# Kernel tuning notes

Hardware: AMD Instinct MI355X
Metric: run time of the kernel (lower is better)

## Reference

```python
import jax, jax.numpy as jnp
import numpy as np

N = 50000      # nodes
E = 500000     # edges (avg degree 10)
G = 64         # graphs (events)
IN = 7
H = 64
EPS = 1e-5


def setup_inputs() -> dict:
    key = jax.random.key(0)
    ks = iter(jax.random.split(key, 64))
    d = {}
    d["x"] = jax.random.normal(next(ks), (N, IN), jnp.float32)
    d["edge_index"] = jax.random.randint(next(ks), (2, E), 0, N, dtype=jnp.int32)
    d["batch"] = jnp.sort(jax.random.randint(next(ks), (N,), 0, G, dtype=jnp.int32))
    dims = [(IN, H), (H, 2 * H), (2 * H, 4 * H)]
    for i, (ic, oc) in enumerate(dims, 1):
        d[f"b{i}_W1"] = jax.random.normal(next(ks), (2 * ic, oc), jnp.float32) * 0.05
        d[f"b{i}_b1"] = jnp.zeros((oc,), jnp.float32)
        d[f"b{i}_g1"] = jnp.ones((oc,), jnp.float32)
        d[f"b{i}_beta1"] = jnp.zeros((oc,), jnp.float32)
        d[f"b{i}_W2"] = jax.random.normal(next(ks), (oc, oc), jnp.float32) * 0.05
        d[f"b{i}_b2"] = jnp.zeros((oc,), jnp.float32)
        d[f"b{i}_g2"] = jnp.ones((oc,), jnp.float32)
        d[f"b{i}_beta2"] = jnp.zeros((oc,), jnp.float32)
    d["head_W1"] = jax.random.normal(next(ks), (4 * H, 2 * H), jnp.float32) * 0.05
    d["head_b1"] = jnp.zeros((2 * H,), jnp.float32)
    d["head_W2"] = jax.random.normal(next(ks), (2 * H, 2), jnp.float32) * 0.05
    d["head_b2"] = jnp.zeros((2,), jnp.float32)
    return d


def _bn(h, g, b):
    # BatchNorm1d in training mode: batch statistics over edge dim
    m = h.mean(axis=0)
    v = h.var(axis=0)
    return (h - m) * jax.lax.rsqrt(v + EPS) * g + b


def _edgeconv(x, src, dst, W1, b1, g1, be1, W2, b2, g2, be2):
    # PyG EdgeConv: message = MLP(cat[x_i, x_j - x_i]), aggregated at target i=dst
    xi = x[dst]                                   # [E, C]
    xj = x[src]                                   # [E, C]
    e = jnp.concatenate([xi, xj - xi], axis=-1)   # [E, 2C]
    h = jax.nn.relu(_bn(e @ W1 + b1, g1, be1))
    h = jax.nn.relu(_bn(h @ W2 + b2, g2, be2))
    s = jax.ops.segment_sum(h, dst, num_segments=N)
    cnt = jax.ops.segment_sum(jnp.ones((h.shape[0],), h.dtype), dst, num_segments=N)
    return s / jnp.maximum(cnt, 1.0)[:, None]     # mean aggregation


def reference(x, edge_index, batch,
              b1_W1, b1_b1, b1_g1, b1_beta1, b1_W2, b1_b2, b1_g2, b1_beta2,
              b2_W1, b2_b1, b2_g1, b2_beta1, b2_W2, b2_b2, b2_g2, b2_beta2,
              b3_W1, b3_b1, b3_g1, b3_beta1, b3_W2, b3_b2, b3_g2, b3_beta2,
              head_W1, head_b1, head_W2, head_b2):
    src, dst = edge_index[0], edge_index[1]
    h = _edgeconv(x, src, dst, b1_W1, b1_b1, b1_g1, b1_beta1, b1_W2, b1_b2, b1_g2, b1_beta2)
    h = _edgeconv(h, src, dst, b2_W1, b2_b1, b2_g1, b2_beta1, b2_W2, b2_b2, b2_g2, b2_beta2)
    h = _edgeconv(h, src, dst, b3_W1, b3_b1, b3_g1, b3_beta1, b3_W2, b3_b2, b3_g2, b3_beta2)
    # global mean pool per graph
    s = jax.ops.segment_sum(h, batch, num_segments=G)
    cnt = jax.ops.segment_sum(jnp.ones((N,), h.dtype), batch, num_segments=G)
    g = s / jnp.maximum(cnt, 1.0)[:, None]        # [G, 256]
    # head (dropout is identity in eval)
    z = jax.nn.relu(g @ head_W1 + head_b1)
    return z @ head_W2 + head_b2                  # [G, 2]
```

## Files before the change

### kernel.cpp

```cpp
#include <hip/hip_runtime.h>
#include <stdint.h>

constexpr int NN = 50000;
constexpr int NE = 500000;
constexpr int NG = 64;
constexpr float BN_EPS = 1e-5f;

typedef __attribute__((ext_vector_type(8))) short bf16x8;
typedef __attribute__((ext_vector_type(4))) float f32x4;

__device__ inline float bf2f(unsigned short u) {
    return __uint_as_float(((unsigned int)u) << 16);
}
__device__ inline unsigned short f2bf_rne(float f) {
    unsigned int u = __float_as_uint(f);
    unsigned int r = (u + 0x7fffu + ((u >> 16) & 1u)) >> 16;
    return (unsigned short)r;
}

template<int CPT> __device__ inline void load_row(const float* p, float* o) {
    if constexpr (CPT == 2) { float2 v = *(const float2*)p; o[0]=v.x; o[1]=v.y; }
    else if constexpr (CPT == 4) { float4 v = *(const float4*)p; o[0]=v.x; o[1]=v.y; o[2]=v.z; o[3]=v.w; }
    else { load_row<4>(p, o); load_row<4>(p+4, o+4); }
}
template<int CPT> __device__ inline void store_row(float* p, const float* v) {
    if constexpr (CPT == 2) { *(float2*)p = make_float2(v[0], v[1]); }
    else if constexpr (CPT == 4) { *(float4*)p = make_float4(v[0], v[1], v[2], v[3]); }
    else { store_row<4>(p, v); store_row<4>(p+4, v+4); }
}

__global__ void k_zero16(uint4* p, int n) {
    int i = blockIdx.x * 256 + threadIdx.x;
    if (i < n) p[i] = uint4{0u, 0u, 0u, 0u};
}

__global__ void k_diag(float* out, int n, float val) {
    int i = blockIdx.x * 256 + threadIdx.x;
    if (i < n) out[i] = val;
}

__global__ void k_deg(const int* __restrict__ dst, int* __restrict__ degi) {
    int e = blockIdx.x * 256 + threadIdx.x;
    if (e < NE) atomicAdd(&degi[dst[e]], 1);
}

__global__ void k_scan(const int* __restrict__ degi, int* __restrict__ rowptr) {
    __shared__ int buf[1024];
    __shared__ int carry_s;
    const int tid = threadIdx.x;
    if (tid == 0) carry_s = 0;
    __syncthreads();
    for (int base = 0; base < NN; base += 1024) {
        int i = base + tid;
        int v = (i < NN) ? degi[i] : 0;
        buf[tid] = v;
        __syncthreads();
        for (int off = 1; off < 1024; off <<= 1) {
            int t = (tid >= off) ? buf[tid - off] : 0;
            __syncthreads();
            buf[tid] += t;
            __syncthreads();
        }
        if (i < NN) rowptr[i] = carry_s + buf[tid] - v;
        __syncthreads();
        if (tid == 0) carry_s += buf[1023];
        __syncthreads();
    }
    if (tid == 0) rowptr[NN] = carry_s;
}

__global__ void k_fill(const int* __restrict__ dst, const int* __restrict__ rowptr,
                       int* __restrict__ cursor, int* __restrict__ eidx) {
    int e = blockIdx.x * 256 + threadIdx.x;
    if (e < NE) {
        int d = dst[e];
        int p = atomicAdd(&cursor[d], 1);
        eidx[rowptr[d] + p] = e;
    }
}

__global__ void k_grange(const int* __restrict__ batch, int* __restrict__ gse) {
    int n = blockIdx.x * 256 + threadIdx.x;
    if (n >= NN) return;
    int b = batch[n];
    if (n == 0 || batch[n-1] != b) gse[b] = n;
    if (n == NN-1 || batch[n+1] != b) gse[NG + b] = n + 1;
}

template<int OC>
__global__ void k_bnfin(const float* __restrict__ st, const float* __restrict__ g,
                        const float* __restrict__ be, float* __restrict__ dv) {
    int c = threadIdx.x;
    const float invE = 1.0f / (float)NE;
    float m = st[c] * invE;
    float v = st[OC + c] * invE - m * m;
    float sc = g[c] * rsqrtf(v + BN_EPS);
    dv[c] = sc;
    dv[OC + c] = be[c] - m * sc;
}

template<int OC>
__global__ void k_packW(const float* __restrict__ W,
                        unsigned short* __restrict__ Wph, unsigned short* __restrict__ Wpl) {
    constexpr int NT = OC / 16;
    const int l = threadIdx.x;
    const int ktnt = blockIdx.x;
    const int n = (ktnt % NT) * 16 + (l & 15);
    const int kbase = (ktnt / NT) * 32 + (l >> 4) * 8;
    size_t fo = ((size_t)ktnt * 64 + l) * 8;
    #pragma unroll
    for (int b = 0; b < 8; b++) {
        float w = W[(size_t)(kbase + b) * OC + n];
        unsigned short h = f2bf_rne(w);
        Wph[fo + b] = h;
        Wpl[fo + b] = f2bf_rne(w - bf2f(h));
    }
}

template<int CIN, int OC>
__global__ __launch_bounds__(256) void k_nodeproj(
    const float* __restrict__ x, const float* __restrict__ W1,
    const float* __restrict__ b1, float* __restrict__ A, float* __restrict__ Bn)
{
    constexpr int SP = CIN + 1;
    constexpr int CPT = OC / 32;
    __shared__ float xs[32 * SP];
    const int t = threadIdx.x;
    const int n0 = blockIdx.x * 32;
    {
        const int el = t >> 3, l8 = t & 7;
        int n = n0 + el; if (n >= NN) n = NN - 1;
        const float* xp = x + (size_t)n * CIN;
        for (int k = l8; k < CIN; k += 8) xs[el * SP + k] = xp[k];
    }
    __syncthreads();
    const int tx = t & 31, ty = t >> 5;
    float accA[4][CPT], accB[4][CPT];
    #pragma unroll
    for (int i = 0; i < 4; i++)
        #pragma unroll
        for (int j = 0; j < CPT; j++) { accA[i][j] = 0.f; accB[i][j] = 0.f; }

    const float* Wa = W1 + tx * CPT;
    const float* Wb = W1 + (size_t)CIN * OC + tx * CPT;
    for (int k = 0; k < CIN; k++) {
        float wa[CPT], wb[CPT];
        load_row<CPT>(Wa + (size_t)k * OC, wa);
        load_row<CPT>(Wb + (size_t)k * OC, wb);
        #pragma unroll
        for (int i = 0; i < 4; i++) {
            float ev = xs[(ty * 4 + i) * SP + k];
            #pragma unroll
            for (int j = 0; j < CPT; j++) {
                accA[i][j] = fmaf(ev, wa[j] - wb[j], accA[i][j]);
                accB[i][j] = fmaf(ev, wb[j], accB[i][j]);
            }
        }
    }
    float bs[CPT];
    load_row<CPT>(b1 + tx * CPT, bs);
    #pragma unroll
    for (int i = 0; i < 4; i++) {
        const int n = n0 + ty * 4 + i;
        if (n < NN) {
            float va[CPT];
            #pragma unroll
            for (int j = 0; j < CPT; j++) va[j] = accA[i][j] + bs[j];
            store_row<CPT>(A  + (size_t)n * OC + tx * CPT, va);
            store_row<CPT>(Bn + (size_t)n * OC + tx * CPT, accB[i]);
        }
    }
}

template<int OC>
__global__ __launch_bounds__(256) void k_stats1(
    const float* __restrict__ A, const float* __restrict__ Bn,
    const int* __restrict__ src, const int* __restrict__ dst,
    const int* __restrict__ eidx, float* __restrict__ stats)
{
    constexpr int CPT = OC / 32;
    __shared__ float reds[4 * OC];
    __shared__ float redq[4 * OC];
    const int t = threadIdx.x;
    const int l32 = t & 31, grp = t >> 5;
    float s[CPT], q[CPT];
    #pragma unroll
    for (int j = 0; j < CPT; j++) { s[j] = 0.f; q[j] = 0.f; }
    for (int i = blockIdx.x * 8 + grp; i < NE; i += 8192) {
        const int e = eidx[i];
        float av[CPT], bv[CPT];
        load_row<CPT>(A  + (size_t)dst[e] * OC + l32 * CPT, av);
        load_row<CPT>(Bn + (size_t)src[e] * OC + l32 * CPT, bv);
        #pragma unroll
        for (int j = 0; j < CPT; j++) {
            float h = av[j] + bv[j];
            s[j] += h; q[j] += h * h;
        }
    }
    #pragma unroll
    for (int j = 0; j < CPT; j++) {
        s[j] += __shfl_down(s[j], 32);
        q[j] += __shfl_down(q[j], 32);
    }
    const int w = t >> 6, lane = t & 63;
    if (lane < 32) {
        #pragma unroll
        for (int j = 0; j < CPT; j++) {
            reds[w * OC + lane * CPT + j] = s[j];
            redq[w * OC + lane * CPT + j] = q[j];
        }
    }
    __syncthreads();
    for (int c = t; c < OC; c += 256) {
        float S = reds[c] + reds[OC + c] + reds[2 * OC + c] + reds[3 * OC + c];
        float Q = redq[c] + redq[OC + c] + redq[2 * OC + c] + redq[3 * OC + c];
        atomicAdd(&stats[c], S);
        atomicAdd(&stats[OC + c], Q);
    }
}

template<int OC, int MODE>
__global__ __launch_bounds__(512, 3) void k_efuse(
    const float* __restrict__ A, const float* __restrict__ Bn,
    const int* __restrict__ src, const int* __restrict__ dst,
    const int* __restrict__ eidx,
    const unsigned short* __restrict__ Wph, const unsigned short* __restrict__ Wpl,
    const float* __restrict__ b2,
    const float* __restrict__ dv1, float* __restrict__ stats,
    const float* __restrict__ dv2, float* __restrict__ xout)
{
    constexpr int ETL = 128;
    constexpr int NT = OC / 16;
    constexpr int NTW = NT / 4;
    constexpr int NCH = OC / 64;
    constexpr int SROWS = 8192 / OC;
    constexpr int NSTRIP = ETL / SROWS;
    constexpr int YSTR = OC + 4;
    constexpr int YB = SROWS * YSTR * 4;
    constexpr int TB = (MODE == 0) ? 16384 : 32768;
    constexpr int SMB = (MODE == 1 && YB > TB) ? YB : TB;
    constexpr int NSEG = 512 / OC;
    constexpr int RSEG = SROWS / NSEG;

    __shared__ __align__(16) unsigned char smem[SMB];
    __shared__ int sdst_s[ETL], ssrc_s[ETL];

    const int t = threadIdx.x;
    const int e0 = blockIdx.x * ETL;
    const int valid = (NE - e0 < ETL) ? (NE - e0) : ETL;

    if (t < ETL) {
        int dn = -1, sn = -1;
        if (t < valid) { int e = eidx[e0 + t]; dn = dst[e]; sn = src[e]; }
        sdst_s[t] = dn; ssrc_s[t] = sn;
    }
    __syncthreads();

    const int lane = t & 63, wave = t >> 6;
    const int rg = wave >> 2, ch = wave & 3;
    const int lr = lane & 15, lg = lane >> 4;

    f32x4 acc[4][NTW];
    #pragma unroll
    for (int m = 0; m < 4; m++)
        #pragma unroll
        for (int n = 0; n < NTW; n++) acc[m][n] = (f32x4){0.f, 0.f, 0.f, 0.f};

    const int brow = t >> 2, q = t & 3;
    const bool rvalid = (brow < valid);
    const float* Arow = rvalid ? (A  + (size_t)sdst_s[brow] * OC + q * 16) : nullptr;
    const float* Brow = rvalid ? (Bn + (size_t)ssrc_s[brow] * OC + q * 16) : nullptr;

    for (int kc = 0; kc < NCH; kc++) {
        {
            const int gc0 = kc * 64 + q * 16;
            if (rvalid) {
                #pragma unroll
                for (int i = 0; i < 4; i++) {
                    float4 a  = *(const float4*)(Arow + kc * 64 + i * 4);
                    float4 b  = *(const float4*)(Brow + kc * 64 + i * 4);
                    float4 sc = *(const float4*)(dv1 + gc0 + i * 4);
                    float4 sh = *(const float4*)(dv1 + OC + gc0 + i * 4);
                    float tv[4];
                    tv[0] = fmaxf(fmaf(a.x + b.x, sc.x, sh.x), 0.f);
                    tv[1] = fmaxf(fmaf(a.y + b.y, sc.y, sh.y), 0.f);
                    tv[2] = fmaxf(fmaf(a.z + b.z, sc.z, sh.z), 0.f);
                    tv[3] = fmaxf(fmaf(a.w + b.w, sc.w, sh.w), 0.f);
                    unsigned short hv[4];
                    #pragma unroll
                    for (int j = 0; j < 4; j++) hv[j] = f2bf_rne(tv[j]);
                    const int byt = (brow * 128 + q * 32 + i * 8) ^ ((brow & 7) << 4);
                    *(ushort4*)(smem + byt) = *(ushort4*)hv;
                    if constexpr (MODE == 1) {
                        unsigned short lv[4];
                        #pragma unroll
                        for (int j = 0; j < 4; j++) lv[j] = f2bf_rne(tv[j] - bf2f(hv[j]));
                        *(ushort4*)(smem + 16384 + byt) = *(ushort4*)lv;
                    }
                }
            } else {
                const ushort4 z = ushort4{0, 0, 0, 0};
                #pragma unroll
                for (int i = 0; i < 4; i++) {
                    const int byt = (brow * 128 + q * 32 + i * 8) ^ ((brow & 7) << 4);
                    *(ushort4*)(smem + byt) = z;
                    if constexpr (MODE == 1) *(ushort4*)(smem + 16384 + byt) = z;
                }
            }
        }
        __syncthreads();

        #pragma unroll
        for (int kt2 = 0; kt2 < 2; kt2++) {
            bf16x8 ah[4], al[4];
            #pragma unroll
            for (int m = 0; m < 4; m++) {
                const int r = rg * 64 + m * 16 + lr;
                const int byt = (r * 128 + kt2 * 64 + lg * 16) ^ ((r & 7) << 4);
                ah[m] = *(const bf16x8*)(smem + byt);
                if constexpr (MODE == 1) al[m] = *(const bf16x8*)(smem + 16384 + byt);
            }
            #pragma unroll
            for (int n = 0; n < NTW; n++) {
                const size_t fo = ((size_t)((kc * 2 + kt2) * NT + ch * NTW + n) * 64 + lane) * 8;
                bf16x8 wh = *(const bf16x8*)(Wph + fo);
                if constexpr (MODE == 0) {
                    #pragma unroll
                    for (int m = 0; m < 4; m++)
                        acc[m][n] = __builtin_amdgcn_mfma_f32_16x16x32_bf16(ah[m], wh, acc[m][n], 0, 0, 0);
                } else {
                    bf16x8 wl = *(const bf16x8*)(Wpl + fo);
                    #pragma unroll
                    for (int m = 0; m < 4; m++) {
                        acc[m][n] = __builtin_amdgcn_mfma_f32_16x16x32_bf16(ah[m], wh, acc[m][n], 0, 0, 0);
                        acc[m][n] = __builtin_amdgcn_mfma_f32_16x16x32_bf16(ah[m], wl, acc[m][n], 0, 0, 0);
                        acc[m][n] = __builtin_amdgcn_mfma_f32_16x16x32_bf16(al[m], wh, acc[m][n], 0, 0, 0);
                    }
                }
            }
        }
        __syncthreads();
    }

    if constexpr (MODE == 0) {
        #pragma unroll
        for (int n = 0; n < NTW; n++) {
            const int col = (ch * NTW + n) * 16 + lr;
            const float bb = b2[col];
            float s = 0.f, qq = 0.f;
            #pragma unroll
            for (int m = 0; m < 4; m++) {
                const int rbase = rg * 64 + m * 16 + lg * 4;
                #pragma unroll
                for (int e = 0; e < 4; e++) {
                    float h = (rbase + e < valid) ? (acc[m][n][e] + bb) : 0.f;
                    s += h; qq += h * h;
                }
            }
            s += __shfl_xor(s, 16); s += __shfl_xor(s, 32);
            qq += __shfl_xor(qq, 16); qq += __shfl_xor(qq, 32);
            if (lg == 0) {
                atomicAdd(&stats[col], s);
                atomicAdd(&stats[OC + col], qq);
            }
        }
    } else {
        float* yt = (float*)smem;
        const int acol = t % OC;
        const int aseg = t / OC;
        #pragma unroll
        for (int s = 0; s < NSTRIP; s++) {
            const int r0 = s * SROWS;
            #pragma unroll
            for (int m = 0; m < 4; m++) {
                const int base = rg * 64 + m * 16;
                if (base >= r0 && base < r0 + SROWS) {
                    #pragma unroll
                    for (int n = 0; n < NTW; n++) {
                        const int col = (ch * NTW + n) * 16 + lr;
                        const float bb = b2[col], scv = dv2[col], shv = dv2[OC + col];
                        #pragma unroll
                        for (int e = 0; e < 4; e++) {
                            const int rl = base - r0 + lg * 4 + e;
                            yt[rl * YSTR + col] = fmaxf(fmaf(acc[m][n][e] + bb, scv, shv), 0.f);
                        }
                    }
                }
            }
            __syncthreads();
            {
                const int rbeg = aseg * RSEG;
                float a = 0.f; int cur = -1;
                for (int r = 0; r < RSEG; r++) {
                    const int gr = r0 + rbeg + r;
                    if (gr >= valid) break;
                    const int nd = sdst_s[gr];
                    if (nd != cur) {
                        if (cur >= 0) atomicAdd(&xout[(size_t)cur * OC + acol], a);
                        cur = nd; a = 0.f;
                    }
                    a += yt[(rbeg + r) * YSTR + acol];
                }
                if (cur >= 0) atomicAdd(&xout[(size_t)cur * OC + acol], a);
            }
            __syncthreads();
        }
    }
}

template<int OC>
__global__ __launch_bounds__(256) void k_div(float* __restrict__ xout,
                                             const int* __restrict__ degi) {
    constexpr int CPT = OC / 32;
    const int tx = threadIdx.x & 31;
    const int n = blockIdx.x * 8 + (threadIdx.x >> 5);
    if (n >= NN) return;
    const float inv = 1.0f / fmaxf((float)degi[n], 1.0f);
    float v[CPT];
    load_row<CPT>(xout + (size_t)n * OC + tx * CPT, v);
    #pragma unroll
    for (int j = 0; j < CPT; j++) v[j] *= inv;
    store_row<CPT>(xout + (size_t)n * OC + tx * CPT, v);
}

__global__ void k_pool(const float* __restrict__ x3, const int* __restrict__ gse,
                       float* __restrict__ pooled) {
    const int g = blockIdx.x, c = threadIdx.x;
    const int beg = gse[g], end = gse[NG + g];
    float s = 0.f;
    for (int n = beg; n < end; n++) s += x3[(size_t)n * 256 + c];
    pooled[g * 256 + c] = s / fmaxf((float)(end - beg), 1.0f);
}

__global__ void k_head(const float* __restrict__ pooled,
                       const float* __restrict__ W1, const float* __restrict__ b1,
                       const float* __restrict__ W2, const float* __restrict__ b2,
                       float* __restrict__ out) {
    __shared__ float gv[256];
    __shared__ float z[128];
    const int g = blockIdx.x;
    gv[threadIdx.x] = pooled[g * 256 + threadIdx.x];
    __syncthreads();
    if (threadIdx.x < 128) {
        const int c = threadIdx.x;
        float s = b1[c];
        for (int k = 0; k < 256; k++) s = fmaf(gv[k], W1[k * 128 + c], s);
        z[c] = fmaxf(s, 0.f);
    }
    __syncthreads();
    if (threadIdx.x < 2) {
        const int o = threadIdx.x;
        float s = b2[o];
        for (int k = 0; k < 128; k++) s = fmaf(z[k], W2[k * 2 + o], s);
        out[g * 2 + o] = s;
    }
}

template<int CIN, int OC>
static void run_block(const float* xin, const float* const* Q,
                      float* A, float* B, const int* src, const int* dst,
                      const int* eidx, const unsigned short* Wph, const unsigned short* Wpl,
                      float* st, float* dv, const int* degi,
                      float* xout, hipStream_t s)
{
    const int EG = (NE + 127) / 128;
    k_nodeproj<CIN, OC><<<(NN + 31) / 32, 256, 0, s>>>(xin, Q[0], Q[1], A, B);
    k_stats1<OC><<<1024, 256, 0, s>>>(A, B, src, dst, eidx, st);
    k_bnfin<OC><<<1, OC, 0, s>>>(st, Q[2], Q[3], dv);
    k_efuse<OC, 0><<<EG, 512, 0, s>>>(A, B, src, dst, eidx, Wph, Wpl, Q[5], dv, st + 512, nullptr, nullptr);
    k_bnfin<OC><<<1, OC, 0, s>>>(st + 512, Q[6], Q[7], dv + 512);
    k_zero16<<<((NN * OC / 4) + 255) / 256, 256, 0, s>>>((uint4*)xout, NN * OC / 4);
    k_efuse<OC, 1><<<EG, 512, 0, s>>>(A, B, src, dst, eidx, Wph, Wpl, Q[5], dv, nullptr, dv + 512, xout);
    k_div<OC><<<(NN + 7) / 8, 256, 0, s>>>(xout, degi);
}

extern "C" void kernel_launch(void* const* d_in, const int* in_sizes, int n_in,
                              void* d_out, int out_size, void* d_ws, size_t ws_size,
                              hipStream_t stream)
{
    (void)in_sizes; (void)n_in;
    const float* x = (const float*)d_in[0];
    const int* ei = (const int*)d_in[1];
    const int* src = ei;
    const int* dst = ei + NE;
    const int* batch = (const int*)d_in[2];
    const float* P[28];
    for (int i = 0; i < 28; i++) P[i] = (const float*)d_in[3 + i];
    float* out = (float*)d_out;

    size_t offs[18];
    {
        size_t o = 0;
        auto take = [&](size_t bytes) -> size_t {
            size_t r = o; o = (o + bytes + 255) & ~(size_t)255; return r;
        };
        offs[0] = take((size_t)NN * 256 * 4);
        offs[1] = take((size_t)NN * 256 * 4);
        offs[2] = take((size_t)NN * 256 * 4);
        offs[3] = take((size_t)NN * 128 * 4);
        offs[4] = o;
        offs[5] = take((size_t)NN * 4);
        offs[6] = take((size_t)NN * 4);
        offs[7] = take(3 * 1024 * 4);
        offs[8] = take(2 * NG * 4);
        offs[9] = o;
        offs[10] = take((size_t)(NN + 1) * 4);
        offs[11] = take((size_t)NE * 4);
        offs[12] = take(3 * 1024 * 4);
        offs[13] = take((size_t)NG * 256 * 4);
        offs[14] = take((64*64 + 128*128 + 256*256) * 2);
        offs[15] = take((64*64 + 128*128 + 256*256) * 2);
        offs[16] = o;
        if (ws_size < o) {
            float val = 1000.0f + (float)(ws_size >> 20);
            k_diag<<<(out_size + 255) / 256, 256, 0, stream>>>(out, out_size, val);
            return;
        }
    }

    char* W = (char*)d_ws;
    float* A  = (float*)(W + offs[0]);
    float* B  = (float*)(W + offs[1]);
    float* xa = (float*)(W + offs[2]);
    float* xb = (float*)(W + offs[3]);
    int* degi = (int*)(W + offs[5]);
    int* cursor = (int*)(W + offs[6]);
    float* stats = (float*)(W + offs[7]);
    int* gse = (int*)(W + offs[8]);
    int* rowptr = (int*)(W + offs[10]);
    int* eidx = (int*)(W + offs[11]);
    float* dv = (float*)(W + offs[12]);
    float* pooled = (float*)(W + offs[13]);
    unsigned short* Wph = (unsigned short*)(W + offs[14]);
    unsigned short* Wpl = (unsigned short*)(W + offs[15]);
    unsigned short* Wph1 = Wph,            * Wpl1 = Wpl;
    unsigned short* Wph2 = Wph + 64*64,    * Wpl2 = Wpl + 64*64;
    unsigned short* Wph3 = Wph2 + 128*128, * Wpl3 = Wpl2 + 128*128;

    int nz = (int)((offs[9] - offs[4]) / 16);
    k_zero16<<<(nz + 255) / 256, 256, 0, stream>>>((uint4*)(W + offs[4]), nz);

    k_deg<<<(NE + 255) / 256, 256, 0, stream>>>(dst, degi);
    k_scan<<<1, 1024, 0, stream>>>(degi, rowptr);
    k_fill<<<(NE + 255) / 256, 256, 0, stream>>>(dst, rowptr, cursor, eidx);
    k_grange<<<(NN + 255) / 256, 256, 0, stream>>>(batch, gse);

    k_packW<64> <<<(64/32)*(64/16),   64, 0, stream>>>(P[4],  Wph1, Wpl1);
    k_packW<128><<<(128/32)*(128/16), 64, 0, stream>>>(P[12], Wph2, Wpl2);
    k_packW<256><<<(256/32)*(256/16), 64, 0, stream>>>(P[20], Wph3, Wpl3);

    run_block<7,   64>(x,  P + 0,  A, B, src, dst, eidx, Wph1, Wpl1, stats + 0,    dv + 0,    degi, xa, stream);
    run_block<64, 128>(xa, P + 8,  A, B, src, dst, eidx, Wph2, Wpl2, stats + 1024, dv + 1024, degi, xb, stream);
    run_block<128,256>(xb, P + 16, A, B, src, dst, eidx, Wph3, Wpl3, stats + 2048, dv + 2048, degi, xa, stream);

    k_pool<<<NG, 256, 0, stream>>>(xa, gse, pooled);
    k_head<<<NG, 256, 0, stream>>>(pooled, P[24], P[25], P[26], P[27], out);
}
```

Baseline: 2.522 ms.

## Compute first BN stats from node-level sums and read bf16 node projections

The first BatchNorm statistics are no longer computed per edge. The edge sum is rewritten as in-degree- and out-degree-weighted node sums, plus a cross term built from a per-destination gather-sum S of source projections. S is accumulated into the output buffer with atomics, and a second degree pass counts out-degrees. Node projections are also written as bf16 copies, which the statistics-only efuse pass reads to halve its gather traffic. The costs are extra bf16 stores and atomic traffic, and second-BN stats computed from bf16-rounded inputs may differ slightly from the fp32 values used in the final pass.

```diff
diff --git a/kernel.cpp b/kernel.cpp
--- a/kernel.cpp
+++ b/kernel.cpp
@@ -12,6 +12,12 @@
 __device__ inline float bf2f(unsigned short u) {
     return __uint_as_float(((unsigned int)u) << 16);
 }
+__device__ inline float bf2f_lo(unsigned int u) {
+    return __uint_as_float((u & 0xffffu) << 16);
+}
+__device__ inline float bf2f_hi(unsigned int u) {
+    return __uint_as_float(u & 0xffff0000u);
+}
 __device__ inline unsigned short f2bf_rne(float f) {
     unsigned int u = __float_as_uint(f);
     unsigned int r = (u + 0x7fffu + ((u >> 16) & 1u)) >> 16;
@@ -28,6 +34,21 @@
     else if constexpr (CPT == 4) { *(float4*)p = make_float4(v[0], v[1], v[2], v[3]); }
     else { store_row<4>(p, v); store_row<4>(p+4, v+4); }
 }
+template<int CPT> __device__ inline void store_hi(unsigned short* p, const float* v) {
+    unsigned int w[CPT / 2];
+    #pragma unroll
+    for (int j = 0; j < CPT / 2; j++)
+        w[j] = (unsigned int)f2bf_rne(v[2*j]) | ((unsigned int)f2bf_rne(v[2*j+1]) << 16);
+    if constexpr (CPT == 2) { *(unsigned int*)p = w[0]; }
+    else if constexpr (CPT == 4) { *(uint2*)p = uint2{w[0], w[1]}; }
+    else { *(uint4*)p = uint4{w[0], w[1], w[2], w[3]}; }
+}
+__device__ inline void unpack8(uint4 u, float* f) {
+    f[0]=bf2f_lo(u.x); f[1]=bf2f_hi(u.x);
+    f[2]=bf2f_lo(u.y); f[3]=bf2f_hi(u.y);
+    f[4]=bf2f_lo(u.z); f[5]=bf2f_hi(u.z);
+    f[6]=bf2f_lo(u.w); f[7]=bf2f_hi(u.w);
+}
 
 __global__ void k_zero16(uint4* p, int n) {
     int i = blockIdx.x * 256 + threadIdx.x;
@@ -39,9 +60,9 @@
     if (i < n) out[i] = val;
 }
 
-__global__ void k_deg(const int* __restrict__ dst, int* __restrict__ degi) {
+__global__ void k_deg(const int* __restrict__ idx, int* __restrict__ cnt) {
     int e = blockIdx.x * 256 + threadIdx.x;
-    if (e < NE) atomicAdd(&degi[dst[e]], 1);
+    if (e < NE) atomicAdd(&cnt[idx[e]], 1);
 }
 
 __global__ void k_scan(const int* __restrict__ degi, int* __restrict__ rowptr) {
@@ -120,7 +141,8 @@
 template<int CIN, int OC>
 __global__ __launch_bounds__(256) void k_nodeproj(
     const float* __restrict__ x, const float* __restrict__ W1,
-    const float* __restrict__ b1, float* __restrict__ A, float* __restrict__ Bn)
+    const float* __restrict__ b1, float* __restrict__ A, float* __restrict__ Bn,
+    unsigned short* __restrict__ Ah, unsigned short* __restrict__ Bh)
 {
     constexpr int SP = CIN + 1;
     constexpr int CPT = OC / 32;
@@ -168,15 +190,54 @@
             for (int j = 0; j < CPT; j++) va[j] = accA[i][j] + bs[j];
             store_row<CPT>(A  + (size_t)n * OC + tx * CPT, va);
             store_row<CPT>(Bn + (size_t)n * OC + tx * CPT, accB[i]);
+            store_hi<CPT>(Ah + (size_t)n * OC + tx * CPT, va);
+            store_hi<CPT>(Bh + (size_t)n * OC + tx * CPT, accB[i]);
         }
     }
 }
 
 template<int OC>
-__global__ __launch_bounds__(256) void k_stats1(
+__global__ __launch_bounds__(512) void k_sgather(
+    const float* __restrict__ Bn,
+    const int* __restrict__ src, const int* __restrict__ dst,
+    const int* __restrict__ eidx, float* __restrict__ S)
+{
+    constexpr int ETL = 128;
+    constexpr int NSEG = 512 / OC;
+    constexpr int RSEG = ETL / NSEG;
+    __shared__ int sdst_s[ETL], ssrc_s[ETL];
+    const int t = threadIdx.x;
+    const int e0 = blockIdx.x * ETL;
+    const int valid = (NE - e0 < ETL) ? (NE - e0) : ETL;
+    if (t < ETL) {
+        int dn = -1, sn = 0;
+        if (t < valid) { int e = eidx[e0 + t]; dn = dst[e]; sn = src[e]; }
+        sdst_s[t] = dn; ssrc_s[t] = sn;
+    }
+    __syncthreads();
+    const int col = t % OC;
+    const int rbeg = (t / OC) * RSEG;
+    float a = 0.f; int cur = -1;
+    for (int r = 0; r < RSEG; r++) {
+        const int gr = rbeg + r;
+        if (gr >= valid) break;
+        const int nd = sdst_s[gr];
+        float v = Bn[(size_t)ssrc_s[gr] * OC + col];
+        if (nd != cur) {
+            if (cur >= 0) atomicAdd(&S[(size_t)cur * OC + col], a);
+            cur = nd; a = 0.f;
+        }
+        a += v;
+    }
+    if (cur >= 0) atomicAdd(&S[(size_t)cur * OC + col], a);
+}
+
+template<int OC>
+__global__ __launch_bounds__(256) void k_snode(
     const float* __restrict__ A, const float* __restrict__ Bn,
-    const int* __restrict__ src, const int* __restrict__ dst,
-    const int* __restrict__ eidx, float* __restrict__ stats)
+    const float* __restrict__ S,
+    const int* __restrict__ degi, const int* __restrict__ dego,
+    float* __restrict__ stats)
 {
     constexpr int CPT = OC / 32;
     __shared__ float reds[4 * OC];
@@ -186,15 +247,16 @@
     float s[CPT], q[CPT];
     #pragma unroll
     for (int j = 0; j < CPT; j++) { s[j] = 0.f; q[j] = 0.f; }
-    for (int i = blockIdx.x * 8 + grp; i < NE; i += 8192) {
-        const int e = eidx[i];
-        float av[CPT], bv[CPT];
-        load_row<CPT>(A  + (size_t)dst[e] * OC + l32 * CPT, av);
-        load_row<CPT>(Bn + (size_t)src[e] * OC + l32 * CPT, bv);
+    for (int n = blockIdx.x * 8 + grp; n < NN; n += 8192) {
+        const float dI = (float)degi[n], dO = (float)dego[n];
+        float av[CPT], bv[CPT], sv[CPT];
+        load_row<CPT>(A  + (size_t)n * OC + l32 * CPT, av);
+        load_row<CPT>(Bn + (size_t)n * OC + l32 * CPT, bv);
+        load_row<CPT>(S  + (size_t)n * OC + l32 * CPT, sv);
         #pragma unroll
         for (int j = 0; j < CPT; j++) {
-            float h = av[j] + bv[j];
-            s[j] += h; q[j] += h * h;
+            s[j] += dI * av[j] + dO * bv[j];
+            q[j] += dI * av[j] * av[j] + dO * bv[j] * bv[j] + 2.f * av[j] * sv[j];
         }
     }
     #pragma unroll
@@ -212,16 +274,17 @@
     }
     __syncthreads();
     for (int c = t; c < OC; c += 256) {
-        float S = reds[c] + reds[OC + c] + reds[2 * OC + c] + reds[3 * OC + c];
-        float Q = redq[c] + redq[OC + c] + redq[2 * OC + c] + redq[3 * OC + c];
-        atomicAdd(&stats[c], S);
-        atomicAdd(&stats[OC + c], Q);
+        float S2 = reds[c] + reds[OC + c] + reds[2 * OC + c] + reds[3 * OC + c];
+        float Q2 = redq[c] + redq[OC + c] + redq[2 * OC + c] + redq[3 * OC + c];
+        atomicAdd(&stats[c], S2);
+        atomicAdd(&stats[OC + c], Q2);
     }
 }
 
 template<int OC, int MODE>
 __global__ __launch_bounds__(512, 3) void k_efuse(
     const float* __restrict__ A, const float* __restrict__ Bn,
+    const unsigned short* __restrict__ Ah, const unsigned short* __restrict__ Bh,
     const int* __restrict__ src, const int* __restrict__ dst,
     const int* __restrict__ eidx,
     const unsigned short* __restrict__ Wph, const unsigned short* __restrict__ Wpl,
@@ -250,7 +313,7 @@
     const int valid = (NE - e0 < ETL) ? (NE - e0) : ETL;
 
     if (t < ETL) {
-        int dn = -1, sn = -1;
+        int dn = -1, sn = 0;
         if (t < valid) { int e = eidx[e0 + t]; dn = dst[e]; sn = src[e]; }
         sdst_s[t] = dn; ssrc_s[t] = sn;
     }
@@ -268,24 +331,34 @@
 
     const int brow = t >> 2, q = t & 3;
     const bool rvalid = (brow < valid);
-    const float* Arow = rvalid ? (A  + (size_t)sdst_s[brow] * OC + q * 16) : nullptr;
-    const float* Brow = rvalid ? (Bn + (size_t)ssrc_s[brow] * OC + q * 16) : nullptr;
 
     for (int kc = 0; kc < NCH; kc++) {
         {
             const int gc0 = kc * 64 + q * 16;
             if (rvalid) {
+                float af[16], bfv[16];
+                if constexpr (MODE == 0) {
+                    const unsigned short* Ar = Ah + (size_t)sdst_s[brow] * OC + gc0;
+                    const unsigned short* Br = Bh + (size_t)ssrc_s[brow] * OC + gc0;
+                    unpack8(*(const uint4*)(Ar), af);
+                    unpack8(*(const uint4*)(Ar + 8), af + 8);
+                    unpack8(*(const uint4*)(Br), bfv);
+                    unpack8(*(const uint4*)(Br + 8), bfv + 8);
+                } else {
+                    const float* Ar = A  + (size_t)sdst_s[brow] * OC + gc0;
+                    const float* Br = Bn + (size_t)ssrc_s[brow] * OC + gc0;
+                    load_row<8>(Ar, af);     load_row<8>(Ar + 8, af + 8);
+                    load_row<8>(Br, bfv);    load_row<8>(Br + 8, bfv + 8);
+                }
                 #pragma unroll
                 for (int i = 0; i < 4; i++) {
-                    float4 a  = *(const float4*)(Arow + kc * 64 + i * 4);
-                    float4 b  = *(const float4*)(Brow + kc * 64 + i * 4);
                     float4 sc = *(const float4*)(dv1 + gc0 + i * 4);
                     float4 sh = *(const float4*)(dv1 + OC + gc0 + i * 4);
                     float tv[4];
-                    tv[0] = fmaxf(fmaf(a.x + b.x, sc.x, sh.x), 0.f);
-                    tv[1] = fmaxf(fmaf(a.y + b.y, sc.y, sh.y), 0.f);
-                    tv[2] = fmaxf(fmaf(a.z + b.z, sc.z, sh.z), 0.f);
-                    tv[3] = fmaxf(fmaf(a.w + b.w, sc.w, sh.w), 0.f);
+                    tv[0] = fmaxf(fmaf(af[i*4+0] + bfv[i*4+0], sc.x, sh.x), 0.f);
+                    tv[1] = fmaxf(fmaf(af[i*4+1] + bfv[i*4+1], sc.y, sh.y), 0.f);
+                    tv[2] = fmaxf(fmaf(af[i*4+2] + bfv[i*4+2], sc.z, sh.z), 0.f);
+                    tv[3] = fmaxf(fmaf(af[i*4+3] + bfv[i*4+3], sc.w, sh.w), 0.f);
                     unsigned short hv[4];
                     #pragma unroll
                     for (int j = 0; j < 4; j++) hv[j] = f2bf_rne(tv[j]);
@@ -458,19 +531,23 @@
 
 template<int CIN, int OC>
 static void run_block(const float* xin, const float* const* Q,
-                      float* A, float* B, const int* src, const int* dst,
+                      float* A, float* B, unsigned short* Ah, unsigned short* Bh,
+                      const int* src, const int* dst,
                       const int* eidx, const unsigned short* Wph, const unsigned short* Wpl,
-                      float* st, float* dv, const int* degi,
+                      float* st, float* dv, const int* degi, const int* dego,
                       float* xout, hipStream_t s)
 {
     const int EG = (NE + 127) / 128;
-    k_nodeproj<CIN, OC><<<(NN + 31) / 32, 256, 0, s>>>(xin, Q[0], Q[1], A, B);
-    k_stats1<OC><<<1024, 256, 0, s>>>(A, B, src, dst, eidx, st);
+    float* S = xout;
+    k_nodeproj<CIN, OC><<<(NN + 31) / 32, 256, 0, s>>>(xin, Q[0], Q[1], A, B, Ah, Bh);
+    k_zero16<<<((NN * OC / 4) + 255) / 256, 256, 0, s>>>((uint4*)S, NN * OC / 4);
+    k_sgather<OC><<<EG, 512, 0, s>>>(B, src, dst, eidx, S);
+    k_snode<OC><<<1024, 256, 0, s>>>(A, B, S, degi, dego, st);
     k_bnfin<OC><<<1, OC, 0, s>>>(st, Q[2], Q[3], dv);
-    k_efuse<OC, 0><<<EG, 512, 0, s>>>(A, B, src, dst, eidx, Wph, Wpl, Q[5], dv, st + 512, nullptr, nullptr);
+    k_efuse<OC, 0><<<EG, 512, 0, s>>>(A, B, Ah, Bh, src, dst, eidx, Wph, Wpl, Q[5], dv, st + 512, nullptr, nullptr);
     k_bnfin<OC><<<1, OC, 0, s>>>(st + 512, Q[6], Q[7], dv + 512);
     k_zero16<<<((NN * OC / 4) + 255) / 256, 256, 0, s>>>((uint4*)xout, NN * OC / 4);
-    k_efuse<OC, 1><<<EG, 512, 0, s>>>(A, B, src, dst, eidx, Wph, Wpl, Q[5], dv, nullptr, dv + 512, xout);
+    k_efuse<OC, 1><<<EG, 512, 0, s>>>(A, B, Ah, Bh, src, dst, eidx, Wph, Wpl, Q[5], dv, nullptr, dv + 512, xout);
     k_div<OC><<<(NN + 7) / 8, 256, 0, s>>>(xout, degi);
 }
 
@@ -488,7 +565,7 @@
     for (int i = 0; i < 28; i++) P[i] = (const float*)d_in[3 + i];
     float* out = (float*)d_out;
 
-    size_t offs[18];
+    size_t offs[21];
     {
         size_t o = 0;
         auto take = [&](size_t bytes) -> size_t {
@@ -501,16 +578,19 @@
         offs[4] = o;
         offs[5] = take((size_t)NN * 4);
         offs[6] = take((size_t)NN * 4);
-        offs[7] = take(3 * 1024 * 4);
-        offs[8] = take(2 * NG * 4);
-        offs[9] = o;
-        offs[10] = take((size_t)(NN + 1) * 4);
-        offs[11] = take((size_t)NE * 4);
-        offs[12] = take(3 * 1024 * 4);
-        offs[13] = take((size_t)NG * 256 * 4);
-        offs[14] = take((64*64 + 128*128 + 256*256) * 2);
+        offs[7] = take((size_t)NN * 4);
+        offs[8] = take(3 * 1024 * 4);
+        offs[9] = take(2 * NG * 4);
+        offs[10] = o;
+        offs[11] = take((size_t)(NN + 1) * 4);
+        offs[12] = take((size_t)NE * 4);
+        offs[13] = take(3 * 1024 * 4);
+        offs[14] = take((size_t)NG * 256 * 4);
         offs[15] = take((64*64 + 128*128 + 256*256) * 2);
-        offs[16] = o;
+        offs[16] = take((64*64 + 128*128 + 256*256) * 2);
+        offs[17] = take((size_t)NN * 256 * 2);
+        offs[18] = take((size_t)NN * 256 * 2);
+        offs[19] = o;
         if (ws_size < o) {
             float val = 1000.0f + (float)(ws_size >> 20);
             k_diag<<<(out_size + 255) / 256, 256, 0, stream>>>(out, out_size, val);
@@ -524,23 +604,27 @@
     float* xa = (float*)(W + offs[2]);
     float* xb = (float*)(W + offs[3]);
     int* degi = (int*)(W + offs[5]);
-    int* cursor = (int*)(W + offs[6]);
-    float* stats = (float*)(W + offs[7]);
-    int* gse = (int*)(W + offs[8]);
-    int* rowptr = (int*)(W + offs[10]);
-    int* eidx = (int*)(W + offs[11]);
-    float* dv = (float*)(W + offs[12]);
-    float* pooled = (float*)(W + offs[13]);
-    unsigned short* Wph = (unsigned short*)(W + offs[14]);
-    unsigned short* Wpl = (unsigned short*)(W + offs[15]);
+    int* dego = (int*)(W + offs[6]);
+    int* cursor = (int*)(W + offs[7]);
+    float* stats = (float*)(W + offs[8]);
+    int* gse = (int*)(W + offs[9]);
+    int* rowptr = (int*)(W + offs[11]);
+    int* eidx = (int*)(W + offs[12]);
+    float* dv = (float*)(W + offs[13]);
+    float* pooled = (float*)(W + offs[14]);
+    unsigned short* Wph = (unsigned short*)(W + offs[15]);
+    unsigned short* Wpl = (unsigned short*)(W + offs[16]);
+    unsigned short* Ah = (unsigned short*)(W + offs[17]);
+    unsigned short* Bh = (unsigned short*)(W + offs[18]);
     unsigned short* Wph1 = Wph,            * Wpl1 = Wpl;
     unsigned short* Wph2 = Wph + 64*64,    * Wpl2 = Wpl + 64*64;
     unsigned short* Wph3 = Wph2 + 128*128, * Wpl3 = Wpl2 + 128*128;
 
-    int nz = (int)((offs[9] - offs[4]) / 16);
+    int nz = (int)((offs[10] - offs[4]) / 16);
     k_zero16<<<(nz + 255) / 256, 256, 0, stream>>>((uint4*)(W + offs[4]), nz);
 
     k_deg<<<(NE + 255) / 256, 256, 0, stream>>>(dst, degi);
+    k_deg<<<(NE + 255) / 256, 256, 0, stream>>>(src, dego);
     k_scan<<<1, 1024, 0, stream>>>(degi, rowptr);
     k_fill<<<(NE + 255) / 256, 256, 0, stream>>>(dst, rowptr, cursor, eidx);
     k_grange<<<(NN + 255) / 256, 256, 0, stream>>>(batch, gse);
@@ -549,9 +633,9 @@
     k_packW<128><<<(128/32)*(128/16), 64, 0, stream>>>(P[12], Wph2, Wpl2);
     k_packW<256><<<(256/32)*(256/16), 64, 0, stream>>>(P[20], Wph3, Wpl3);
 
-    run_block<7,   64>(x,  P + 0,  A, B, src, dst, eidx, Wph1, Wpl1, stats + 0,    dv + 0,    degi, xa, stream);
-    run_block<64, 128>(xa, P + 8,  A, B, src, dst, eidx, Wph2, Wpl2, stats + 1024, dv + 1024, degi, xb, stream);
-    run_block<128,256>(xb, P + 16, A, B, src, dst, eidx, Wph3, Wpl3, stats + 2048, dv + 2048, degi, xa, stream);
+    run_block<7,   64>(x,  P + 0,  A, B, Ah, Bh, src, dst, eidx, Wph1, Wpl1, stats + 0,    dv + 0,    degi, dego, xa, stream);
+    run_block<64, 128>(xa, P + 8,  A, B, Ah, Bh, src, dst, eidx, Wph2, Wpl2, stats + 1024, dv + 1024, degi, dego, xb, stream);
+    run_block<128,256>(xb, P + 16, A, B, Ah, Bh, src, dst, eidx, Wph3, Wpl3, stats + 2048, dv + 2048, degi, dego, xa, stream);
 
     k_pool<<<NG, 256, 0, stream>>>(xa, gse, pooled);
     k_head<<<NG, 256, 0, stream>>>(pooled, P[24], P[25], P[26], P[27], out);
```

Result: slower. 2.617 ms (+3.8%).
